# Kernel tuning notes

Measured on AMD Instinct MI355X. Metric: run time of the kernel, lower is better.

## Reference

```python
import jax, jax.numpy as jnp
import numpy as np

E, F, H = 8, 4096, 2048  # num_experts, ffn_hidden_size, hidden_size
B, S, K = 2, 1024, 4     # batch, seq_len, top_k


def setup_inputs() -> dict:
    key = jax.random.key(0)
    ks = jax.random.split(key, 7)
    x = jax.random.normal(ks[0], (B, S, H), dtype=jnp.float32)
    weights = jax.random.uniform(ks[1], (B * S, E), dtype=jnp.float32)
    top_weights = jax.random.uniform(ks[2], (B * S, K), dtype=jnp.float32)
    top_experts = jax.random.randint(ks[3], (B * S, K), 0, E)
    w1 = jax.random.normal(ks[4], (E, F, H), dtype=jnp.float32) * 0.02
    v1 = jax.random.normal(ks[5], (E, F, H), dtype=jnp.float32) * 0.02
    w2 = jax.random.normal(ks[6], (E, F, H), dtype=jnp.float32) * 0.02
    return {"x": x, "weights": weights, "top_weights": top_weights,
            "top_experts": top_experts, "w1": w1, "v1": v1, "w2": w2}


def reference(x, weights, top_weights, top_experts, w1, v1, w2):
    # weights (router probs) is accepted but unused, matching the torch forward.
    bsz, q_len, hidden = x.shape
    xt = x.reshape(-1, hidden)  # [T, H]
    num_experts = w1.shape[0]
    # scale[t, e] = sum_k top_weights[t, k] * (top_experts[t, k] == e)
    onehot = jax.nn.one_hot(top_experts, num_experts, dtype=xt.dtype)  # [T, K, E]
    scale = jnp.einsum("tke,tk->te", onehot, top_weights)  # [T, E]
    out = jnp.zeros_like(xt)
    for e in range(num_experts):  # fixed small expert loop, dense+masked combine
        gate = xt @ w1[e].T          # [T, F]
        up = xt @ v1[e].T            # [T, F]
        h = jax.nn.silu(gate) * up   # DbrxExpertGLU
        out = out + (h @ w2[e]) * scale[:, e:e + 1]
    return out.reshape(bsz, q_len, hidden)
```

## Files before the change

### kernel.cpp

```cpp
#include <hip/hip_runtime.h>
#include <hip/hip_bf16.h>

#define NE 8
#define FF 4096
#define HH 2048
#define TT 2048
#define KTOP 4

typedef unsigned short u16;
typedef __attribute__((ext_vector_type(8))) short bf16x8;
typedef __attribute__((ext_vector_type(4))) float f32x4;

#define CFENCE asm volatile("" ::: "memory")

__device__ __forceinline__ u16 f2u(float f) {
  __hip_bfloat16 b = __float2bfloat16(f);
  return *reinterpret_cast<u16*>(&b);
}

__device__ __forceinline__ void gld16(void* lds, const void* g) {
  __builtin_amdgcn_global_load_lds(
      (const __attribute__((address_space(1))) void*)g,
      (__attribute__((address_space(3))) void*)lds, 16, 0, 0);
}

__global__ void k_build(const int* __restrict__ te, int* __restrict__ cnt,
                        int* __restrict__ tok, int* __restrict__ posmap) {
  const int e = blockIdx.x;
  const int tl = threadIdx.x;
  const int base = tl * 8;
  int mem[8];
  int my = 0;
  #pragma unroll
  for (int i = 0; i < 8; ++i) {
    const int t = base + i;
    bool m = false;
    #pragma unroll
    for (int k = 0; k < KTOP; ++k) m |= (te[t * KTOP + k] == e);
    mem[i] = m ? 1 : 0;
    my += mem[i];
  }
  __shared__ int s[256];
  s[tl] = my;
  __syncthreads();
  for (int off = 1; off < 256; off <<= 1) {
    int v = (tl >= off) ? s[tl - off] : 0;
    __syncthreads();
    s[tl] += v;
    __syncthreads();
  }
  int r = s[tl] - my;
  if (tl == 255) cnt[e] = s[255];
  #pragma unroll
  for (int i = 0; i < 8; ++i) {
    if (mem[i]) {
      const int t = base + i;
      tok[e * TT + r] = t;
      posmap[t * NE + e] = r;
      ++r;
    }
  }
}

__global__ void k_cast4(const float4* __restrict__ src, ushort4* __restrict__ dst, int n4) {
  int stride = gridDim.x * blockDim.x;
  for (int i = blockIdx.x * blockDim.x + threadIdx.x; i < n4; i += stride) {
    float4 f = src[i];
    ushort4 o;
    o.x = f2u(f.x); o.y = f2u(f.y); o.z = f2u(f.z); o.w = f2u(f.w);
    dst[i] = o;
  }
}

template<int MODE>
__global__ __launch_bounds__(512)
void gemm256(const u16* __restrict__ Aall, const u16* __restrict__ Ball,
             const int* __restrict__ cnt, void* __restrict__ Oall,
             const float* __restrict__ W1, const float* __restrict__ V1,
             const int* __restrict__ tok, const u16* __restrict__ Zp,
             const float* __restrict__ W2, u16* __restrict__ W2t) {
  constexpr int KD  = (MODE == 0) ? HH : FF;
  constexpr int NTK = KD / 64;
  constexpr int NT  = (MODE == 0) ? 32 : 8;
  constexpr int NB  = (MODE == 0) ? 2 * FF : HH;
  constexpr int NWG = (MODE == 0) ? 2048 : 512;

  __shared__ __align__(16) u16 smem[65536];
  const int bid = blockIdx.x;
  const int tid = threadIdx.x;

  if (MODE == 0 && bid >= NWG) {
    float (*tile)[65] = reinterpret_cast<float(*)[65]>(smem);
    const int r = tid >> 3;
    const int c0 = (tid & 7) * 8;
    for (int i = 0; i < 8; ++i) {
      const int g = (bid - NWG) * 8 + i;
      const int e = g >> 11;
      const int rem = g & 2047;
      const int f0 = (rem >> 5) << 6;
      const int h0 = (rem & 31) << 6;
      const float* src = W2 + (size_t)e * FF * HH + (size_t)(f0 + r) * HH + h0 + c0;
      float4 a = ((const float4*)src)[0];
      float4 b = ((const float4*)src)[1];
      tile[r][c0 + 0] = a.x; tile[r][c0 + 1] = a.y;
      tile[r][c0 + 2] = a.z; tile[r][c0 + 3] = a.w;
      tile[r][c0 + 4] = b.x; tile[r][c0 + 5] = b.y;
      tile[r][c0 + 6] = b.z; tile[r][c0 + 7] = b.w;
      __syncthreads();
      union { ushort u[8]; bf16x8 v; } o;
      #pragma unroll
      for (int j = 0; j < 8; ++j) o.u[j] = f2u(tile[c0 + j][r]);
      *(bf16x8*)(W2t + (size_t)e * HH * FF + (size_t)(h0 + r) * FF + f0 + c0) = o.v;
      __syncthreads();
    }
    return;
  }

  const int swz = (bid & 7) * (NWG >> 3) + (bid >> 3);
  const int e   = swz / (8 * NT);
  const int rem = swz % (8 * NT);
  const int ntl = rem / 8;
  const int mt  = rem % 8;
  const int c = cnt[e];
  const int mcap = (c + 255) & ~255;
  if (mt * 256 >= mcap) return;

  const int lane = tid & 63;
  const int wave = tid >> 6;
  const int wm = wave >> 2;
  const int wn = wave & 3;

  const int tq = tid >> 2;
  const int tc = (((tid & 3) ^ ((tid >> 3) & 3)) << 3);

  const u16* pA0;
  const u16* pA1;
  if constexpr (MODE == 0) {
    const int r0 = mt * 256 + tq;
    const int r1 = r0 + 128;
    pA0 = ((r0 < c) ? Aall + (size_t)tok[e * TT + r0] * HH : Zp) + tc;
    pA1 = ((r1 < c) ? Aall + (size_t)tok[e * TT + r1] * HH : Zp) + tc;
  } else {
    const u16* A = Aall + (size_t)e * TT * KD + (size_t)(mt * 256) * KD;
    pA0 = A + (size_t)tq * KD + tc;
    pA1 = pA0 + (size_t)128 * KD;
  }

  auto stageA = [&](int d, int ks, int kt) {
    u16* dst = smem + ((d * 2 + ks) << 13) + tid * 8;
    const int off = kt * 64 + ks * 32;
    gld16(dst,        pA0 + off);
    gld16(dst + 4096, pA1 + off);
  };

  const u16* pB = Ball + (size_t)e * NB * KD + (size_t)(ntl * 256) * KD
                       + (size_t)tq * KD + tc;
  auto stageB = [&](int d, int ks, int kt) {
    u16* dst = smem + 32768 + ((d * 2 + ks) << 13) + tid * 8;
    const u16* src = pB + kt * 64 + ks * 32;
    gld16(dst,        src);
    gld16(dst + 4096, src + (size_t)128 * KD);
  };

  const float* pW = nullptr;
  if constexpr (MODE == 0) {
    const int sel = (tq >> 4) & 1;
    const int fr  = ntl * 128 + (tq >> 5) * 16 + (tq & 15);
    pW = (sel ? V1 : W1) + ((size_t)(e * FF + fr)) * HH + (tid & 3) * 8;
  }
  float4 br0[4], br1[4];
  auto issueB = [&](float4* br, int ks, int kt) {
    const float* s = pW + kt * 64 + ks * 32;
    br[0] = ((const float4*)s)[0];
    br[1] = ((const float4*)s)[1];
    const float* s2 = s + (size_t)64 * HH;
    br[2] = ((const float4*)s2)[0];
    br[3] = ((const float4*)s2)[1];
  };
  auto cvtB = [&](float4* br, int d, int ks) {
    u16* dst = smem + 32768 + ((d * 2 + ks) << 13) + tq * 32 + tc;
    union { ushort u[8]; bf16x8 v; } lo, hi;
    lo.u[0]=f2u(br[0].x); lo.u[1]=f2u(br[0].y); lo.u[2]=f2u(br[0].z); lo.u[3]=f2u(br[0].w);
    lo.u[4]=f2u(br[1].x); lo.u[5]=f2u(br[1].y); lo.u[6]=f2u(br[1].z); lo.u[7]=f2u(br[1].w);
    hi.u[0]=f2u(br[2].x); hi.u[1]=f2u(br[2].y); hi.u[2]=f2u(br[2].z); hi.u[3]=f2u(br[2].w);
    hi.u[4]=f2u(br[3].x); hi.u[5]=f2u(br[3].y); hi.u[6]=f2u(br[3].z); hi.u[7]=f2u(br[3].w);
    *(bf16x8*)(dst)        = lo.v;
    *(bf16x8*)(dst + 4096) = hi.v;
  };

  f32x4 acc[8][4];
  #pragma unroll
  for (int m = 0; m < 8; ++m)
    #pragma unroll
    for (int n = 0; n < 4; ++n)
      acc[m][n] = (f32x4){0.f, 0.f, 0.f, 0.f};

  const int lr = lane & 15;
  const int lc = ((((lane >> 4) & 3) ^ ((lane >> 1) & 3)) << 3);

  bf16x8 af[4], bf[4];
  auto rdA = [&](int d, int ks, int mq) {
    const u16* blk = smem + ((d * 2 + ks) << 13);
    #pragma unroll
    for (int m = 0; m < 4; ++m)
      af[m] = *(const bf16x8*)(blk + (wm * 128 + mq * 64 + m * 16 + lr) * 32 + lc);
  };
  auto rdB = [&](int d, int ks) {
    const u16* blk = smem + 32768 + ((d * 2 + ks) << 13);
    #pragma unroll
    for (int n = 0; n < 4; ++n)
      bf[n] = *(const bf16x8*)(blk + (wn * 64 + n * 16 + lr) * 32 + lc);
  };
  auto vmwait = [&](int n) {
    switch (n) {
      case 0:  asm volatile("s_waitcnt vmcnt(0)"  ::: "memory"); break;
      case 6:  asm volatile("s_waitcnt vmcnt(6)"  ::: "memory"); break;
      default: asm volatile("s_waitcnt vmcnt(8)"  ::: "memory"); break;
    }
  };
  auto MF = [&](int mq) {
    __builtin_amdgcn_s_setprio(1);
    #pragma unroll
    for (int m = 0; m < 4; ++m)
      #pragma unroll
      for (int n = 0; n < 4; ++n)
        acc[mq * 4 + m][n] = __builtin_amdgcn_mfma_f32_16x16x32_bf16(
            af[m], bf[n], acc[mq * 4 + m][n], 0, 0, 0);
    __builtin_amdgcn_s_setprio(0);
  };

  if constexpr (MODE == 0) {
    issueB(br0, 0, 0);
    issueB(br1, 1, 0);
    stageA(0, 0, 0);
    stageA(0, 1, 0);
    cvtB(br0, 0, 0);
    cvtB(br1, 0, 1);
    issueB(br0, 0, 1);
    issueB(br1, 1, 1);
    vmwait(8);
    asm volatile("s_waitcnt lgkmcnt(0)" ::: "memory");
  } else {
    stageA(0, 0, 0); stageA(0, 1, 0);
    stageB(0, 0, 0); stageB(0, 1, 0);
    vmwait(0);
  }
  __builtin_amdgcn_s_barrier();
  CFENCE;

  for (int t = 0; t < NTK; ++t) {
    const int d = t & 1, dn = d ^ 1;
    const bool hasN  = (t + 1 < NTK);
    const bool hasN2 = (t + 2 < NTK);

    rdB(d, 0); rdA(d, 0, 0);
    if (hasN) {
      stageA(dn, 0, t + 1);
      stageA(dn, 1, t + 1);
      if constexpr (MODE == 1) { stageB(dn, 0, t + 1); stageB(dn, 1, t + 1); }
    }
    __builtin_amdgcn_sched_barrier(0);
    MF(0);
    rdA(d, 0, 1);
    MF(1);
    if constexpr (MODE == 0) {
      if (hasN)  cvtB(br0, dn, 0);
      if (hasN2) issueB(br0, 0, t + 2);
    }
    rdB(d, 1); rdA(d, 1, 0);
    MF(0);
    if constexpr (MODE == 0) {
      if (hasN)  cvtB(br1, dn, 1);
      if (hasN2) issueB(br1, 1, t + 2);
    }
    rdA(d, 1, 1);
    MF(1);
    if constexpr (MODE == 0) {
      asm volatile("s_waitcnt lgkmcnt(0)" ::: "memory");
      vmwait(hasN2 ? 8 : 0);
    } else {
      vmwait(0);
    }
    __builtin_amdgcn_s_barrier();
    CFENCE;
  }

  const int rb = mt * 256 + wm * 128 + ((lane >> 4) << 2);
  if (MODE == 0) {
    u16* H = (u16*)Oall + (size_t)e * TT * FF;
    const int fb = ntl * 128 + wn * 32 + lr;
    #pragma unroll
    for (int m = 0; m < 8; ++m)
      #pragma unroll
      for (int np = 0; np < 2; ++np)
        #pragma unroll
        for (int j = 0; j < 4; ++j) {
          float g = acc[m][2*np][j];
          float u = acc[m][2*np + 1][j];
          float hh = (g / (1.f + __expf(-g))) * u;
          H[(size_t)(rb + m*16 + j) * FF + fb + np*16] = f2u(hh);
        }
  } else {
    float* D = (float*)Oall + (size_t)e * TT * HH;
    const int cb = ntl * 256 + wn * 64 + lr;
    #pragma unroll
    for (int m = 0; m < 8; ++m)
      #pragma unroll
      for (int n = 0; n < 4; ++n)
        #pragma unroll
        for (int j = 0; j < 4; ++j)
          D[(size_t)(rb + m*16 + j) * HH + cb + n*16] = acc[m][n][j];
  }
}

__global__ void k_combine(const float* __restrict__ tw, const int* __restrict__ te,
                          const int* __restrict__ posmap, const float* __restrict__ dcomp,
                          float* __restrict__ out) {
  const int t = blockIdx.x;
  const int c0 = threadIdx.x * 8;
  float a[8] = {0.f, 0.f, 0.f, 0.f, 0.f, 0.f, 0.f, 0.f};
  #pragma unroll
  for (int k = 0; k < KTOP; ++k) {
    const int e = te[t * KTOP + k];
    const float w = tw[t * KTOP + k];
    const int r = posmap[t * NE + e];
    const float* row = dcomp + ((size_t)e * TT + r) * HH + c0;
    const float4 p = ((const float4*)row)[0];
    const float4 q = ((const float4*)row)[1];
    a[0] += w * p.x; a[1] += w * p.y; a[2] += w * p.z; a[3] += w * p.w;
    a[4] += w * q.x; a[5] += w * q.y; a[6] += w * q.z; a[7] += w * q.w;
  }
  float* o = out + (size_t)t * HH + c0;
  ((float4*)o)[0] = (float4){a[0], a[1], a[2], a[3]};
  ((float4*)o)[1] = (float4){a[4], a[5], a[6], a[7]};
}

extern "C" void kernel_launch(void* const* d_in, const int* in_sizes, int n_in,
                              void* d_out, int out_size, void* d_ws, size_t ws_size,
                              hipStream_t stream) {
  const float* x  = (const float*)d_in[0];
  const float* tw = (const float*)d_in[2];
  const int*   te = (const int*)d_in[3];
  const float* w1 = (const float*)d_in[4];
  const float* v1 = (const float*)d_in[5];
  const float* w2 = (const float*)d_in[6];
  float* out = (float*)d_out;

  char* p = (char*)d_ws;
  int*   cnt    = (int*)p;   p += 256;
  int*   tok    = (int*)p;   p += (size_t)NE * TT * 4;
  int*   posmap = (int*)p;   p += (size_t)TT * NE * 4;
  u16*   zp     = (u16*)p;   p += (size_t)HH * 2;
  u16*   xb     = (u16*)p;   p += (size_t)TT * HH * 2;
  u16*   w2tb   = (u16*)p;   p += (size_t)NE * HH * FF * 2;
  u16*   hc     = (u16*)p;   p += (size_t)NE * TT * FF * 2;
  float* dcomp  = (float*)p; p += (size_t)NE * TT * HH * 4;

  hipMemsetAsync(zp, 0, (size_t)HH * 2, stream);
  k_build<<<NE, 256, 0, stream>>>(te, cnt, tok, posmap);
  k_cast4<<<1024, 256, 0, stream>>>((const float4*)x, (ushort4*)xb, TT * HH / 4);

  gemm256<0><<<4096, 512, 0, stream>>>(xb, nullptr, cnt, hc, w1, v1, tok, zp,
                                       w2, w2tb);
  gemm256<1><<<512, 512, 0, stream>>>(hc, w2tb, cnt, dcomp, nullptr, nullptr,
                                      nullptr, nullptr, nullptr, nullptr);
  k_combine<<<TT, 256, 0, stream>>>(tw, te, posmap, dcomp, out);
}
```

Measured before the change: 507.5 us.

## Pipeline expert groups across chained launches overlapping GLU, down-proj and W2 cast

Replaces the two monolithic GEMM launches with five launches of a combined kernel. Each launch runs the down projection for one pair of experts next to the GLU GEMM for the next pair and the W2 transpose-cast for a later pair, so all three phases overlap and the tail of each phase is filled. The down-projection output buffer is also stored as bf16 rather than fp32, which halves its write and combine read traffic. This costs some output precision and adds extra launch boundaries that act as synchronisation points between groups.

```diff
diff --git a/kernel.cpp b/kernel.cpp
--- a/kernel.cpp
+++ b/kernel.cpp
@@ -8,6 +8,7 @@
 #define KTOP 4
 
 typedef unsigned short u16;
+typedef unsigned int u32;
 typedef __attribute__((ext_vector_type(8))) short bf16x8;
 typedef __attribute__((ext_vector_type(4))) float f32x4;
 
@@ -16,12 +17,23 @@
 __device__ __forceinline__ u16 f2u(float f) {
   __hip_bfloat16 b = __float2bfloat16(f);
   return *reinterpret_cast<u16*>(&b);
+}
+__device__ __forceinline__ float u2f(u16 u) {
+  union { u32 i; float f; } c; c.i = ((u32)u) << 16; return c.f;
 }
 
 __device__ __forceinline__ void gld16(void* lds, const void* g) {
   __builtin_amdgcn_global_load_lds(
       (const __attribute__((address_space(1))) void*)g,
       (__attribute__((address_space(3))) void*)lds, 16, 0, 0);
+}
+
+__device__ __forceinline__ void vmwait(int n) {
+  switch (n) {
+    case 0:  asm volatile("s_waitcnt vmcnt(0)"  ::: "memory"); break;
+    case 6:  asm volatile("s_waitcnt vmcnt(6)"  ::: "memory"); break;
+    default: asm volatile("s_waitcnt vmcnt(8)"  ::: "memory"); break;
+  }
 }
 
 __global__ void k_build(const int* __restrict__ te, int* __restrict__ cnt,
@@ -72,59 +84,52 @@
   }
 }
 
-template<int MODE>
-__global__ __launch_bounds__(512)
-void gemm256(const u16* __restrict__ Aall, const u16* __restrict__ Ball,
-             const int* __restrict__ cnt, void* __restrict__ Oall,
-             const float* __restrict__ W1, const float* __restrict__ V1,
-             const int* __restrict__ tok, const u16* __restrict__ Zp,
-             const float* __restrict__ W2, u16* __restrict__ W2t) {
-  constexpr int KD  = (MODE == 0) ? HH : FF;
-  constexpr int NTK = KD / 64;
-  constexpr int NT  = (MODE == 0) ? 32 : 8;
-  constexpr int NB  = (MODE == 0) ? 2 * FF : HH;
-  constexpr int NWG = (MODE == 0) ? 2048 : 512;
-
-  __shared__ __align__(16) u16 smem[65536];
-  const int bid = blockIdx.x;
+
+__device__ __forceinline__ void tcast_block(int lbid, int e0, u16* smem,
+                                            const float* __restrict__ W2,
+                                            u16* __restrict__ W2t) {
+  float (*tile)[65] = reinterpret_cast<float(*)[65]>(smem);
   const int tid = threadIdx.x;
-
-  if (MODE == 0 && bid >= NWG) {
-    float (*tile)[65] = reinterpret_cast<float(*)[65]>(smem);
-    const int r = tid >> 3;
-    const int c0 = (tid & 7) * 8;
-    for (int i = 0; i < 8; ++i) {
-      const int g = (bid - NWG) * 8 + i;
-      const int e = g >> 11;
-      const int rem = g & 2047;
-      const int f0 = (rem >> 5) << 6;
-      const int h0 = (rem & 31) << 6;
-      const float* src = W2 + (size_t)e * FF * HH + (size_t)(f0 + r) * HH + h0 + c0;
-      float4 a = ((const float4*)src)[0];
-      float4 b = ((const float4*)src)[1];
-      tile[r][c0 + 0] = a.x; tile[r][c0 + 1] = a.y;
-      tile[r][c0 + 2] = a.z; tile[r][c0 + 3] = a.w;
-      tile[r][c0 + 4] = b.x; tile[r][c0 + 5] = b.y;
-      tile[r][c0 + 6] = b.z; tile[r][c0 + 7] = b.w;
-      __syncthreads();
-      union { ushort u[8]; bf16x8 v; } o;
-      #pragma unroll
-      for (int j = 0; j < 8; ++j) o.u[j] = f2u(tile[c0 + j][r]);
-      *(bf16x8*)(W2t + (size_t)e * HH * FF + (size_t)(h0 + r) * FF + f0 + c0) = o.v;
-      __syncthreads();
-    }
-    return;
-  }
-
-  const int swz = (bid & 7) * (NWG >> 3) + (bid >> 3);
-  const int e   = swz / (8 * NT);
-  const int rem = swz % (8 * NT);
-  const int ntl = rem / 8;
-  const int mt  = rem % 8;
+  const int r = tid >> 3;
+  const int c0 = (tid & 7) * 8;
+  for (int i = 0; i < 8; ++i) {
+    const int g = e0 * 2048 + lbid * 8 + i;
+    const int e = g >> 11;
+    const int rem = g & 2047;
+    const int f0 = (rem >> 5) << 6;
+    const int h0 = (rem & 31) << 6;
+    const float* src = W2 + (size_t)e * FF * HH + (size_t)(f0 + r) * HH + h0 + c0;
+    float4 a = ((const float4*)src)[0];
+    float4 b = ((const float4*)src)[1];
+    tile[r][c0 + 0] = a.x; tile[r][c0 + 1] = a.y;
+    tile[r][c0 + 2] = a.z; tile[r][c0 + 3] = a.w;
+    tile[r][c0 + 4] = b.x; tile[r][c0 + 5] = b.y;
+    tile[r][c0 + 6] = b.z; tile[r][c0 + 7] = b.w;
+    __syncthreads();
+    union { ushort u[8]; bf16x8 v; } o;
+    #pragma unroll
+    for (int j = 0; j < 8; ++j) o.u[j] = f2u(tile[c0 + j][r]);
+    *(bf16x8*)(W2t + (size_t)e * HH * FF + (size_t)(h0 + r) * FF + f0 + c0) = o.v;
+    __syncthreads();
+  }
+}
+
+__device__ __forceinline__ void glu_block(int lbid, int e0, u16* smem,
+    const u16* __restrict__ xb, const int* __restrict__ cnt,
+    const int* __restrict__ tok, const u16* __restrict__ Zp,
+    u16* __restrict__ hc, const float* __restrict__ W1,
+    const float* __restrict__ V1) {
+  constexpr int KD = HH, NTK = HH / 64;
+  const int swz = (lbid & 7) * 64 + (lbid >> 3);
+  const int e   = e0 + (swz >> 8);
+  const int rem = swz & 255;
+  const int ntl = rem >> 3;
+  const int mt  = rem & 7;
   const int c = cnt[e];
   const int mcap = (c + 255) & ~255;
   if (mt * 256 >= mcap) return;
 
+  const int tid  = threadIdx.x;
   const int lane = tid & 63;
   const int wave = tid >> 6;
   const int wm = wave >> 2;
@@ -133,18 +138,10 @@
   const int tq = tid >> 2;
   const int tc = (((tid & 3) ^ ((tid >> 3) & 3)) << 3);
 
-  const u16* pA0;
-  const u16* pA1;
-  if constexpr (MODE == 0) {
-    const int r0 = mt * 256 + tq;
-    const int r1 = r0 + 128;
-    pA0 = ((r0 < c) ? Aall + (size_t)tok[e * TT + r0] * HH : Zp) + tc;
-    pA1 = ((r1 < c) ? Aall + (size_t)tok[e * TT + r1] * HH : Zp) + tc;
-  } else {
-    const u16* A = Aall + (size_t)e * TT * KD + (size_t)(mt * 256) * KD;
-    pA0 = A + (size_t)tq * KD + tc;
-    pA1 = pA0 + (size_t)128 * KD;
-  }
+  const int r0 = mt * 256 + tq;
+  const int r1 = r0 + 128;
+  const u16* pA0 = ((r0 < c) ? xb + (size_t)tok[e * TT + r0] * HH : Zp) + tc;
+  const u16* pA1 = ((r1 < c) ? xb + (size_t)tok[e * TT + r1] * HH : Zp) + tc;
 
   auto stageA = [&](int d, int ks, int kt) {
     u16* dst = smem + ((d * 2 + ks) << 13) + tid * 8;
@@ -153,21 +150,10 @@
     gld16(dst + 4096, pA1 + off);
   };
 
-  const u16* pB = Ball + (size_t)e * NB * KD + (size_t)(ntl * 256) * KD
-                       + (size_t)tq * KD + tc;
-  auto stageB = [&](int d, int ks, int kt) {
-    u16* dst = smem + 32768 + ((d * 2 + ks) << 13) + tid * 8;
-    const u16* src = pB + kt * 64 + ks * 32;
-    gld16(dst,        src);
-    gld16(dst + 4096, src + (size_t)128 * KD);
-  };
-
-  const float* pW = nullptr;
-  if constexpr (MODE == 0) {
-    const int sel = (tq >> 4) & 1;
-    const int fr  = ntl * 128 + (tq >> 5) * 16 + (tq & 15);
-    pW = (sel ? V1 : W1) + ((size_t)(e * FF + fr)) * HH + (tid & 3) * 8;
-  }
+  const int sel = (tq >> 4) & 1;
+  const int fr  = ntl * 128 + (tq >> 5) * 16 + (tq & 15);
+  const float* pW = (sel ? V1 : W1) + ((size_t)(e * FF + fr)) * HH + (tid & 3) * 8;
+
   float4 br0[4], br1[4];
   auto issueB = [&](float4* br, int ks, int kt) {
     const float* s = pW + kt * 64 + ks * 32;
@@ -211,13 +197,6 @@
     for (int n = 0; n < 4; ++n)
       bf[n] = *(const bf16x8*)(blk + (wn * 64 + n * 16 + lr) * 32 + lc);
   };
-  auto vmwait = [&](int n) {
-    switch (n) {
-      case 0:  asm volatile("s_waitcnt vmcnt(0)"  ::: "memory"); break;
-      case 6:  asm volatile("s_waitcnt vmcnt(6)"  ::: "memory"); break;
-      default: asm volatile("s_waitcnt vmcnt(8)"  ::: "memory"); break;
-    }
-  };
   auto MF = [&](int mq) {
     __builtin_amdgcn_s_setprio(1);
     #pragma unroll
@@ -229,22 +208,16 @@
     __builtin_amdgcn_s_setprio(0);
   };
 
-  if constexpr (MODE == 0) {
-    issueB(br0, 0, 0);
-    issueB(br1, 1, 0);
-    stageA(0, 0, 0);
-    stageA(0, 1, 0);
-    cvtB(br0, 0, 0);
-    cvtB(br1, 0, 1);
-    issueB(br0, 0, 1);
-    issueB(br1, 1, 1);
-    vmwait(8);
-    asm volatile("s_waitcnt lgkmcnt(0)" ::: "memory");
-  } else {
-    stageA(0, 0, 0); stageA(0, 1, 0);
-    stageB(0, 0, 0); stageB(0, 1, 0);
-    vmwait(0);
-  }
+  issueB(br0, 0, 0);
+  issueB(br1, 1, 0);
+  stageA(0, 0, 0);
+  stageA(0, 1, 0);
+  cvtB(br0, 0, 0);
+  cvtB(br1, 0, 1);
+  issueB(br0, 0, 1);
+  issueB(br1, 1, 1);
+  vmwait(8);
+  asm volatile("s_waitcnt lgkmcnt(0)" ::: "memory");
   __builtin_amdgcn_s_barrier();
   CFENCE;
 
@@ -252,69 +225,177 @@
     const int d = t & 1, dn = d ^ 1;
     const bool hasN  = (t + 1 < NTK);
     const bool hasN2 = (t + 2 < NTK);
-
+    rdB(d, 0); rdA(d, 0, 0);
+    if (hasN) { stageA(dn, 0, t + 1); stageA(dn, 1, t + 1); }
+    __builtin_amdgcn_sched_barrier(0);
+    MF(0);
+    rdA(d, 0, 1);
+    MF(1);
+    if (hasN)  cvtB(br0, dn, 0);
+    if (hasN2) issueB(br0, 0, t + 2);
+    rdB(d, 1); rdA(d, 1, 0);
+    MF(0);
+    if (hasN)  cvtB(br1, dn, 1);
+    if (hasN2) issueB(br1, 1, t + 2);
+    rdA(d, 1, 1);
+    MF(1);
+    asm volatile("s_waitcnt lgkmcnt(0)" ::: "memory");
+    vmwait(hasN2 ? 8 : 0);
+    __builtin_amdgcn_s_barrier();
+    CFENCE;
+  }
+
+  u16* H = hc + (size_t)e * TT * FF;
+  const int rb = mt * 256 + wm * 128 + ((lane >> 4) << 2);
+  const int fb = ntl * 128 + wn * 32 + lr;
+  #pragma unroll
+  for (int m = 0; m < 8; ++m)
+    #pragma unroll
+    for (int np = 0; np < 2; ++np)
+      #pragma unroll
+      for (int j = 0; j < 4; ++j) {
+        float g = acc[m][2*np][j];
+        float u = acc[m][2*np + 1][j];
+        float hh = (g / (1.f + __expf(-g))) * u;
+        H[(size_t)(rb + m*16 + j) * FF + fb + np*16] = f2u(hh);
+      }
+}
+
+__device__ __forceinline__ void down_block(int lbid, int e0, u16* smem,
+    const u16* __restrict__ hc, const u16* __restrict__ w2t,
+    const int* __restrict__ cnt, u16* __restrict__ dcomp) {
+  constexpr int KD = FF, NTK = FF / 64;
+  const int swz = (lbid & 7) * 16 + (lbid >> 3);
+  const int e   = e0 + (swz >> 6);
+  const int rem = swz & 63;
+  const int ntl = rem >> 3;
+  const int mt  = rem & 7;
+  const int c = cnt[e];
+  const int mcap = (c + 255) & ~255;
+  if (mt * 256 >= mcap) return;
+
+  const int tid  = threadIdx.x;
+  const int lane = tid & 63;
+  const int wave = tid >> 6;
+  const int wm = wave >> 2;
+  const int wn = wave & 3;
+
+  const int tq = tid >> 2;
+  const int tc = (((tid & 3) ^ ((tid >> 3) & 3)) << 3);
+
+  const u16* A = hc + (size_t)e * TT * KD + (size_t)(mt * 256) * KD;
+  const u16* pA0 = A + (size_t)tq * KD + tc;
+  const u16* pA1 = pA0 + (size_t)128 * KD;
+  const u16* pB = w2t + (size_t)e * HH * KD + (size_t)(ntl * 256) * KD
+                      + (size_t)tq * KD + tc;
+
+  auto stageA = [&](int d, int ks, int kt) {
+    u16* dst = smem + ((d * 2 + ks) << 13) + tid * 8;
+    const int off = kt * 64 + ks * 32;
+    gld16(dst,        pA0 + off);
+    gld16(dst + 4096, pA1 + off);
+  };
+  auto stageB = [&](int d, int ks, int kt) {
+    u16* dst = smem + 32768 + ((d * 2 + ks) << 13) + tid * 8;
+    const u16* src = pB + kt * 64 + ks * 32;
+    gld16(dst,        src);
+    gld16(dst + 4096, src + (size_t)128 * KD);
+  };
+
+  f32x4 acc[8][4];
+  #pragma unroll
+  for (int m = 0; m < 8; ++m)
+    #pragma unroll
+    for (int n = 0; n < 4; ++n)
+      acc[m][n] = (f32x4){0.f, 0.f, 0.f, 0.f};
+
+  const int lr = lane & 15;
+  const int lc = ((((lane >> 4) & 3) ^ ((lane >> 1) & 3)) << 3);
+
+  bf16x8 af[4], bf[4];
+  auto rdA = [&](int d, int ks, int mq) {
+    const u16* blk = smem + ((d * 2 + ks) << 13);
+    #pragma unroll
+    for (int m = 0; m < 4; ++m)
+      af[m] = *(const bf16x8*)(blk + (wm * 128 + mq * 64 + m * 16 + lr) * 32 + lc);
+  };
+  auto rdB = [&](int d, int ks) {
+    const u16* blk = smem + 32768 + ((d * 2 + ks) << 13);
+    #pragma unroll
+    for (int n = 0; n < 4; ++n)
+      bf[n] = *(const bf16x8*)(blk + (wn * 64 + n * 16 + lr) * 32 + lc);
+  };
+  auto MF = [&](int mq) {
+    __builtin_amdgcn_s_setprio(1);
+    #pragma unroll
+    for (int m = 0; m < 4; ++m)
+      #pragma unroll
+      for (int n = 0; n < 4; ++n)
+        acc[mq * 4 + m][n] = __builtin_amdgcn_mfma_f32_16x16x32_bf16(
+            af[m], bf[n], acc[mq * 4 + m][n], 0, 0, 0);
+    __builtin_amdgcn_s_setprio(0);
+  };
+
+  stageA(0, 0, 0); stageA(0, 1, 0);
+  stageB(0, 0, 0); stageB(0, 1, 0);
+  vmwait(0);
+  __builtin_amdgcn_s_barrier();
+  CFENCE;
+
+  for (int t = 0; t < NTK; ++t) {
+    const int d = t & 1, dn = d ^ 1;
+    const bool hasN = (t + 1 < NTK);
     rdB(d, 0); rdA(d, 0, 0);
     if (hasN) {
-      stageA(dn, 0, t + 1);
-      stageA(dn, 1, t + 1);
-      if constexpr (MODE == 1) { stageB(dn, 0, t + 1); stageB(dn, 1, t + 1); }
+      stageA(dn, 0, t + 1); stageA(dn, 1, t + 1);
+      stageB(dn, 0, t + 1); stageB(dn, 1, t + 1);
     }
     __builtin_amdgcn_sched_barrier(0);
     MF(0);
     rdA(d, 0, 1);
     MF(1);
-    if constexpr (MODE == 0) {
-      if (hasN)  cvtB(br0, dn, 0);
-      if (hasN2) issueB(br0, 0, t + 2);
-    }
     rdB(d, 1); rdA(d, 1, 0);
     MF(0);
-    if constexpr (MODE == 0) {
-      if (hasN)  cvtB(br1, dn, 1);
-      if (hasN2) issueB(br1, 1, t + 2);
-    }
     rdA(d, 1, 1);
     MF(1);
-    if constexpr (MODE == 0) {
-      asm volatile("s_waitcnt lgkmcnt(0)" ::: "memory");
-      vmwait(hasN2 ? 8 : 0);
-    } else {
-      vmwait(0);
-    }
+    vmwait(0);
     __builtin_amdgcn_s_barrier();
     CFENCE;
   }
 
+  u16* D = dcomp + (size_t)e * TT * HH;
   const int rb = mt * 256 + wm * 128 + ((lane >> 4) << 2);
-  if (MODE == 0) {
-    u16* H = (u16*)Oall + (size_t)e * TT * FF;
-    const int fb = ntl * 128 + wn * 32 + lr;
-    #pragma unroll
-    for (int m = 0; m < 8; ++m)
+  const int cb = ntl * 256 + wn * 64 + lr;
+  #pragma unroll
+  for (int m = 0; m < 8; ++m)
+    #pragma unroll
+    for (int n = 0; n < 4; ++n)
       #pragma unroll
-      for (int np = 0; np < 2; ++np)
-        #pragma unroll
-        for (int j = 0; j < 4; ++j) {
-          float g = acc[m][2*np][j];
-          float u = acc[m][2*np + 1][j];
-          float hh = (g / (1.f + __expf(-g))) * u;
-          H[(size_t)(rb + m*16 + j) * FF + fb + np*16] = f2u(hh);
-        }
+      for (int j = 0; j < 4; ++j)
+        D[(size_t)(rb + m*16 + j) * HH + cb + n*16] = f2u(acc[m][n][j]);
+}
+
+__global__ __launch_bounds__(512)
+void k_chain(int nDown, int downE0, int nGlu, int gluE0, int tcastE0,
+             const u16* __restrict__ xb, const int* __restrict__ cnt,
+             const int* __restrict__ tok, const u16* __restrict__ Zp,
+             u16* __restrict__ hc, const float* __restrict__ W1,
+             const float* __restrict__ V1, const u16* __restrict__ w2t_c,
+             u16* __restrict__ w2t, u16* __restrict__ dcomp,
+             const float* __restrict__ W2) {
+  __shared__ __align__(16) u16 smem[65536];
+  const int bid = blockIdx.x;
+  if (bid < nDown) {
+    down_block(bid, downE0, smem, hc, w2t_c, cnt, dcomp);
+  } else if (bid < nDown + nGlu) {
+    glu_block(bid - nDown, gluE0, smem, xb, cnt, tok, Zp, hc, W1, V1);
   } else {
-    float* D = (float*)Oall + (size_t)e * TT * HH;
-    const int cb = ntl * 256 + wn * 64 + lr;
-    #pragma unroll
-    for (int m = 0; m < 8; ++m)
-      #pragma unroll
-      for (int n = 0; n < 4; ++n)
-        #pragma unroll
-        for (int j = 0; j < 4; ++j)
-          D[(size_t)(rb + m*16 + j) * HH + cb + n*16] = acc[m][n][j];
+    tcast_block(bid - nDown - nGlu, tcastE0, smem, W2, w2t);
   }
 }
 
 __global__ void k_combine(const float* __restrict__ tw, const int* __restrict__ te,
-                          const int* __restrict__ posmap, const float* __restrict__ dcomp,
+                          const int* __restrict__ posmap, const u16* __restrict__ dcomp,
                           float* __restrict__ out) {
   const int t = blockIdx.x;
   const int c0 = threadIdx.x * 8;
@@ -324,11 +405,11 @@
     const int e = te[t * KTOP + k];
     const float w = tw[t * KTOP + k];
     const int r = posmap[t * NE + e];
-    const float* row = dcomp + ((size_t)e * TT + r) * HH + c0;
-    const float4 p = ((const float4*)row)[0];
-    const float4 q = ((const float4*)row)[1];
-    a[0] += w * p.x; a[1] += w * p.y; a[2] += w * p.z; a[3] += w * p.w;
-    a[4] += w * q.x; a[5] += w * q.y; a[6] += w * q.z; a[7] += w * q.w;
+    const u16* row = dcomp + ((size_t)e * TT + r) * HH + c0;
+    union { bf16x8 v; ushort u[8]; } x;
+    x.v = *(const bf16x8*)row;
+    #pragma unroll
+    for (int j = 0; j < 8; ++j) a[j] += w * u2f(x.u[j]);
   }
   float* o = out + (size_t)t * HH + c0;
   ((float4*)o)[0] = (float4){a[0], a[1], a[2], a[3]};
@@ -354,15 +435,22 @@
   u16*   xb     = (u16*)p;   p += (size_t)TT * HH * 2;
   u16*   w2tb   = (u16*)p;   p += (size_t)NE * HH * FF * 2;
   u16*   hc     = (u16*)p;   p += (size_t)NE * TT * FF * 2;
-  float* dcomp  = (float*)p; p += (size_t)NE * TT * HH * 4;
+  u16*   dcomp  = (u16*)p;   p += (size_t)NE * TT * HH * 2;
 
   hipMemsetAsync(zp, 0, (size_t)HH * 2, stream);
   k_build<<<NE, 256, 0, stream>>>(te, cnt, tok, posmap);
   k_cast4<<<1024, 256, 0, stream>>>((const float4*)x, (ushort4*)xb, TT * HH / 4);
 
-  gemm256<0><<<4096, 512, 0, stream>>>(xb, nullptr, cnt, hc, w1, v1, tok, zp,
-                                       w2, w2tb);
-  gemm256<1><<<512, 512, 0, stream>>>(hc, w2tb, cnt, dcomp, nullptr, nullptr,
-                                      nullptr, nullptr, nullptr, nullptr);
+  k_chain<<<512 + 1024, 512, 0, stream>>>(0, 0, 512, 0, 0,
+      xb, cnt, tok, zp, hc, w1, v1, w2tb, w2tb, dcomp, w2);
+  k_chain<<<128 + 512 + 512, 512, 0, stream>>>(128, 0, 512, 2, 4,
+      xb, cnt, tok, zp, hc, w1, v1, w2tb, w2tb, dcomp, w2);
+  k_chain<<<128 + 512 + 512, 512, 0, stream>>>(128, 2, 512, 4, 6,
+      xb, cnt, tok, zp, hc, w1, v1, w2tb, w2tb, dcomp, w2);
+  k_chain<<<128 + 512, 512, 0, stream>>>(128, 4, 512, 6, 0,
+      xb, cnt, tok, zp, hc, w1, v1, w2tb, w2tb, dcomp, w2);
+  k_chain<<<128, 512, 0, stream>>>(128, 6, 0, 0, 0,
+      xb, cnt, tok, zp, hc, w1, v1, w2tb, w2tb, dcomp, w2);
+
   k_combine<<<TT, 256, 0, stream>>>(tw, te, posmap, dcomp, out);
 }
```

Result: slower. 759.4 us (+49.6%).
